# Performance work log

Measured on AMD Instinct MI355X. Metric: run time of the kernel, lower is better.

The kernel has to match this reference:

```python
import jax, jax.numpy as jnp
import numpy as np

B, SQ, SK, DK, DV = 8, 2048, 2048, 256, 256
EPS = 1e-7  # keras.backend.epsilon()


def setup_inputs() -> dict:
    key = jax.random.key(0)
    kq, kk, kv, km = jax.random.split(key, 4)
    query = jax.random.normal(kq, (B, SQ, DK), dtype=jnp.float32)
    k_ = jax.random.normal(kk, (B, SK, DK), dtype=jnp.float32)
    value = jax.random.normal(kv, (B, SK, DV), dtype=jnp.float32)
    mask = jax.random.uniform(km, (B, SK)) > 0.1
    return {"query": query, "key": k_, "value": value, "mask": mask}


def reference(query, key, value, mask):
    d = query.shape[-1]
    # scores: [B, Sq, Sk]
    e = jnp.einsum('bqd,bkd->bqk', query, key) / jnp.sqrt(jnp.asarray(d, query.dtype))
    # original applies exp(e - max) BEFORE masking (non-standard but faithful)
    e = jnp.exp(e - jnp.max(e, axis=-1, keepdims=True))
    q_len, k_len = query.shape[1], key.shape[1]
    causal = (jnp.arange(k_len)[None, :] <= jnp.arange(q_len)[:, None]).astype(query.dtype)
    e = e * causal[None, :, :]                       # history_only mask
    e = e * mask[:, None, :].astype(query.dtype)     # key padding mask
    a = e / (jnp.sum(e, axis=-1, keepdims=True) + EPS)
    return jnp.einsum('bqk,bkv->bqv', a, value)
```

## Files before the change

kernel.cpp:

```cpp
#include <hip/hip_runtime.h>
#include <hip/hip_bf16.h>

#define B_   8
#define SQ_  2048
#define SK_  2048
#define DK_  256
#define DV_  256

#define KT    32
#define PSTR  40
#define TELEM (KT * DK_)
#define NQB   16

typedef __bf16 bf16x8 __attribute__((ext_vector_type(8)));
typedef float  f32x4  __attribute__((ext_vector_type(4)));

__device__ __forceinline__ void gl_lds16(const void* g, void* l) {
    __builtin_amdgcn_global_load_lds(
        (const __attribute__((address_space(1))) void*)g,
        (__attribute__((address_space(3))) void*)l, 16, 0, 0);
}

__global__ __launch_bounds__(256)
void make_tiles(const float* __restrict__ K, const float* __restrict__ V,
                __bf16* __restrict__ Kt, __bf16* __restrict__ Vt)
{
    const int b = blockIdx.x, t = blockIdx.y;
    const float* ksrc = K + ((size_t)(b * SK_ + t * KT)) * DK_;
    const float* vsrc = V + ((size_t)(b * SK_ + t * KT)) * DV_;

    float4 kf[8];
    #pragma unroll
    for (int it = 0; it < 4; ++it) {
        int ci  = it * 256 + threadIdx.x;
        int dk8 = ci >> 5;
        int key = ci & 31;
        const float* p = ksrc + (size_t)key * DK_ + dk8 * 8;
        kf[it * 2]     = *(const float4*)(p);
        kf[it * 2 + 1] = *(const float4*)(p + 4);
    }
    const int kc8 = threadIdx.x >> 6;
    const int dv4 = threadIdx.x & 63;
    float4 vf[8];
    {
        const float* p = vsrc + (size_t)(kc8 * 8) * DV_ + dv4 * 4;
        #pragma unroll
        for (int j = 0; j < 8; ++j)
            vf[j] = *(const float4*)(p + (size_t)j * DV_);
    }

    __bf16* kout = Kt + ((size_t)(b * 64 + t)) * TELEM;
    #pragma unroll
    for (int it = 0; it < 4; ++it) {
        int ci = it * 256 + threadIdx.x;
        bf16x8 o;
        o[0] = (__bf16)kf[it*2].x;   o[1] = (__bf16)kf[it*2].y;
        o[2] = (__bf16)kf[it*2].z;   o[3] = (__bf16)kf[it*2].w;
        o[4] = (__bf16)kf[it*2+1].x; o[5] = (__bf16)kf[it*2+1].y;
        o[6] = (__bf16)kf[it*2+1].z; o[7] = (__bf16)kf[it*2+1].w;
        *(bf16x8*)(kout + (size_t)ci * 8) = o;
    }
    __bf16* vout = Vt + ((size_t)(b * 64 + t)) * TELEM;
    {
        bf16x8 o0, o1, o2, o3;
        #pragma unroll
        for (int j = 0; j < 8; ++j) {
            o0[j] = (__bf16)vf[j].x; o1[j] = (__bf16)vf[j].y;
            o2[j] = (__bf16)vf[j].z; o3[j] = (__bf16)vf[j].w;
        }
        __bf16* q = vout + (size_t)(kc8 * 256 + dv4 * 4) * 8;
        *(bf16x8*)(q)      = o0;
        *(bf16x8*)(q + 8)  = o1;
        *(bf16x8*)(q + 16) = o2;
        *(bf16x8*)(q + 24) = o3;
    }
}

__global__ __launch_bounds__(256, 2)
void attn_fwd(const float* __restrict__ Qg, const __bf16* __restrict__ Kt,
              const __bf16* __restrict__ Vt, const void* __restrict__ Mv,
              __bf16* __restrict__ Opart, float* __restrict__ Lpart,
              float* __restrict__ Og, int tpc, int slots_pb)
{
    __shared__ __align__(16) __bf16 sK[2][TELEM];
    __shared__ __align__(16) __bf16 sV[2][TELEM];
    __shared__ __align__(16) __bf16 sP[4][32 * PSTR];

    const int tid  = threadIdx.x;
    const int wv   = tid >> 6;
    const int lane = tid & 63;
    const int quad = lane >> 4;
    const int l16  = lane & 15;

    const int b = blockIdx.x;

    int yy = blockIdx.y, qb = 0, s = 0, soff = 0;
    for (int q = NQB - 1; q >= 0; --q) {
        int c = (4 * (q + 1) + tpc - 1) / tpc;
        if (yy < c) { qb = q; s = yy; break; }
        yy -= c;
        if (c > 1) soff += c;
    }
    const int nt = 4 * (qb + 1);
    const int nc = (nt + tpc - 1) / tpc;
    const int t0 = nt * s / nc;
    const int t1 = nt * (s + 1) / nc;

    const int qrow = qb * 128 + wv * 32;

    const unsigned char* Mb = (const unsigned char*)Mv;
    const int*           Mi = (const int*)Mv;
    int nzb = 0;
    {
        const unsigned int* mw = (const unsigned int*)Mv;
        #pragma unroll
        for (int i = 0; i < 32; ++i) {
            unsigned int w = mw[i];
            nzb += ((w & 0x000000ffu) != 0) + ((w & 0x0000ff00u) != 0)
                 + ((w & 0x00ff0000u) != 0) + ((w & 0xff000000u) != 0);
        }
    }
    const bool mask_byte = (nzb > 40);

    bf16x8 qfrag[2][8];
    #pragma unroll
    for (int rs = 0; rs < 2; ++rs) {
        const float* qp = Qg + ((size_t)(b * SQ_ + qrow + rs * 16 + l16)) * DK_ + quad * 8;
        #pragma unroll
        for (int kt = 0; kt < 8; ++kt) {
            float4 f0 = *(const float4*)(qp + kt * 32);
            float4 f1 = *(const float4*)(qp + kt * 32 + 4);
            bf16x8 q;
            q[0] = (__bf16)f0.x; q[1] = (__bf16)f0.y; q[2] = (__bf16)f0.z; q[3] = (__bf16)f0.w;
            q[4] = (__bf16)f1.x; q[5] = (__bf16)f1.y; q[6] = (__bf16)f1.z; q[7] = (__bf16)f1.w;
            qfrag[rs][kt] = q;
        }
    }

    f32x4 oacc[2][16];
    #pragma unroll
    for (int rs = 0; rs < 2; ++rs)
        #pragma unroll
        for (int v = 0; v < 16; ++v) oacc[rs][v] = (f32x4){0.f, 0.f, 0.f, 0.f};
    float lsum[2][4] = {{0.f,0.f,0.f,0.f},{0.f,0.f,0.f,0.f}};

    const __bf16* Kbase = Kt + (size_t)b * 64 * TELEM;
    const __bf16* Vbase = Vt + (size_t)b * 64 * TELEM;
    const size_t  mbase = (size_t)b * SK_;

    {
        const __bf16* kg = Kbase + (size_t)t0 * TELEM;
        const __bf16* vg = Vbase + (size_t)t0 * TELEM;
        #pragma unroll
        for (int r = 0; r < 4; ++r) {
            int ci = r * 256 + tid;
            gl_lds16(kg + (size_t)ci * 8, (char*)&sK[0][0] + ci * 16);
            gl_lds16(vg + (size_t)ci * 8, (char*)&sV[0][0] + ci * 16);
        }
    }
    __syncthreads();

    int cur = 0;
    for (int t = t0; t < t1; ++t) {
        if (t + 1 < t1) {
            const __bf16* kg = Kbase + (size_t)(t + 1) * TELEM;
            const __bf16* vg = Vbase + (size_t)(t + 1) * TELEM;
            #pragma unroll
            for (int r = 0; r < 4; ++r) {
                int ci = r * 256 + tid;
                gl_lds16(kg + (size_t)ci * 8, (char*)&sK[cur ^ 1][0] + ci * 16);
                gl_lds16(vg + (size_t)ci * 8, (char*)&sV[cur ^ 1][0] + ci * 16);
            }
        }

        const int k0 = t * KT;

        f32x4 s00 = {0.f,0.f,0.f,0.f}, s01 = {0.f,0.f,0.f,0.f};
        f32x4 s10 = {0.f,0.f,0.f,0.f}, s11 = {0.f,0.f,0.f,0.f};
        __builtin_amdgcn_s_setprio(1);
        #pragma unroll
        for (int kt = 0; kt < 8; ++kt) {
            bf16x8 b0 = *(const bf16x8*)&sK[cur][(size_t)((kt * 4 + quad) * 32 + l16)      * 8];
            bf16x8 b1 = *(const bf16x8*)&sK[cur][(size_t)((kt * 4 + quad) * 32 + 16 + l16) * 8];
            s00 = __builtin_amdgcn_mfma_f32_16x16x32_bf16(qfrag[0][kt], b0, s00, 0, 0, 0);
            s01 = __builtin_amdgcn_mfma_f32_16x16x32_bf16(qfrag[0][kt], b1, s01, 0, 0, 0);
            s10 = __builtin_amdgcn_mfma_f32_16x16x32_bf16(qfrag[1][kt], b0, s10, 0, 0, 0);
            s11 = __builtin_amdgcn_mfma_f32_16x16x32_bf16(qfrag[1][kt], b1, s11, 0, 0, 0);
        }
        __builtin_amdgcn_s_setprio(0);

        #pragma unroll
        for (int nf = 0; nf < 2; ++nf) {
            int key = k0 + nf * 16 + l16;
            float mk = mask_byte ? (Mb[mbase + key] ? 1.0f : 0.0f)
                                 : (Mi[mbase + key] ? 1.0f : 0.0f);
            #pragma unroll
            for (int rs = 0; rs < 2; ++rs) {
                f32x4 sv = (rs == 0) ? ((nf == 0) ? s00 : s01)
                                     : ((nf == 0) ? s10 : s11);
                #pragma unroll
                for (int i = 0; i < 4; ++i) {
                    int qr = qrow + rs * 16 + quad * 4 + i;
                    float p = __expf(sv[i] * 0.0625f);
                    p = (key <= qr) ? (p * mk) : 0.0f;
                    lsum[rs][i] += p;
                    sP[wv][(rs * 16 + quad * 4 + i) * PSTR + nf * 16 + l16] = (__bf16)p;
                }
            }
        }
        asm volatile("s_waitcnt lgkmcnt(0)" ::: "memory");
        __builtin_amdgcn_wave_barrier();

        {
            bf16x8 pa0 = *(const bf16x8*)&sP[wv][(l16)      * PSTR + quad * 8];
            bf16x8 pa1 = *(const bf16x8*)&sP[wv][(16 + l16) * PSTR + quad * 8];
            __builtin_amdgcn_s_setprio(1);
            #pragma unroll
            for (int vf = 0; vf < 16; ++vf) {
                bf16x8 bv = *(const bf16x8*)&sV[cur][(size_t)(quad * 256 + vf * 16 + l16) * 8];
                oacc[0][vf] = __builtin_amdgcn_mfma_f32_16x16x32_bf16(pa0, bv, oacc[0][vf], 0, 0, 0);
                oacc[1][vf] = __builtin_amdgcn_mfma_f32_16x16x32_bf16(pa1, bv, oacc[1][vf], 0, 0, 0);
            }
            __builtin_amdgcn_s_setprio(0);
        }

        __syncthreads();
        cur ^= 1;
    }

    #pragma unroll
    for (int rs = 0; rs < 2; ++rs)
        #pragma unroll
        for (int i = 0; i < 4; ++i) {
            float v = lsum[rs][i];
            v += __shfl_xor(v, 1);
            v += __shfl_xor(v, 2);
            v += __shfl_xor(v, 4);
            v += __shfl_xor(v, 8);
            lsum[rs][i] = v;
        }

    if (nc == 1) {
        float* op = Og + ((size_t)(b * SQ_ + qb * 128 + wv * 32)) * DV_;
        #pragma unroll
        for (int rs = 0; rs < 2; ++rs)
            #pragma unroll
            for (int i = 0; i < 4; ++i) {
                float inv = 1.0f / (lsum[rs][i] + 1e-7f);
                #pragma unroll
                for (int vf = 0; vf < 16; ++vf)
                    op[(size_t)(rs * 16 + quad * 4 + i) * DV_ + vf * 16 + l16]
                        = oacc[rs][vf][i] * inv;
            }
        return;
    }

    const size_t slot = (size_t)b * slots_pb + soff + s;
    if (l16 == 0) {
        #pragma unroll
        for (int rs = 0; rs < 2; ++rs)
            #pragma unroll
            for (int i = 0; i < 4; ++i)
                Lpart[slot * 128 + wv * 32 + rs * 16 + quad * 4 + i] = lsum[rs][i];
    }
    __bf16* ob = Opart + slot * (size_t)(128 * 256);
    #pragma unroll
    for (int rs = 0; rs < 2; ++rs)
        #pragma unroll
        for (int vf = 0; vf < 16; ++vf)
            #pragma unroll
            for (int i = 0; i < 4; ++i)
                ob[(wv * 32 + rs * 16 + quad * 4 + i) * 256 + vf * 16 + l16]
                    = (__bf16)oacc[rs][vf][i];
}

__global__ __launch_bounds__(512)
void attn_reduce(const __bf16* __restrict__ Opart, const float* __restrict__ Lpart,
                 float* __restrict__ Og, int tpc, int slots_pb)
{
    const int b    = blockIdx.x;
    const int y    = blockIdx.y;
    const int qb64 = y >> 1;
    const int half = y & 1;
    const int qb   = qb64 >> 1;
    const int rowbase = (qb64 & 1) * 64;
    const int chunks = (4 * (qb + 1) + tpc - 1) / tpc;
    if (chunks < 2) return;

    int soff = 0;
    for (int q = NQB - 1; q > qb; --q) {
        int c = (4 * (q + 1) + tpc - 1) / tpc;
        if (c > 1) soff += c;
    }

    const int tid  = threadIdx.x;
    const int row  = tid >> 3;
    const int cg   = tid & 7;

    const size_t sbase = (size_t)b * slots_pb + soff;
    float acc[16];
    #pragma unroll
    for (int i = 0; i < 16; ++i) acc[i] = 0.f;
    float ls = 0.f;

    for (int s = 0; s < chunks; ++s) {
        const __bf16* p = Opart + (sbase + s) * (size_t)(128 * 256)
                        + (size_t)(rowbase + row) * 256 + half * 128 + cg * 16;
        bf16x8 x0 = *(const bf16x8*)(p);
        bf16x8 x1 = *(const bf16x8*)(p + 8);
        #pragma unroll
        for (int e = 0; e < 8; ++e) { acc[e] += (float)x0[e]; acc[8 + e] += (float)x1[e]; }
        ls += Lpart[(sbase + s) * 128 + rowbase + row];
    }
    const float inv = 1.0f / (ls + 1e-7f);
    float* op = Og + ((size_t)b * SQ_ + qb64 * 64 + row) * DV_ + half * 128 + cg * 16;
    #pragma unroll
    for (int v = 0; v < 4; ++v) {
        float4 o;
        o.x = acc[v * 4 + 0] * inv; o.y = acc[v * 4 + 1] * inv;
        o.z = acc[v * 4 + 2] * inv; o.w = acc[v * 4 + 3] * inv;
        *(float4*)(op + v * 4) = o;
    }
}

extern "C" void kernel_launch(void* const* d_in, const int* in_sizes, int n_in,
                              void* d_out, int out_size, void* d_ws, size_t ws_size,
                              hipStream_t stream) {
    const float* Q = (const float*)d_in[0];
    const float* K = (const float*)d_in[1];
    const float* V = (const float*)d_in[2];
    const void*  M = d_in[3];
    float* Out = (float*)d_out;

    __bf16* Ktl = (__bf16*)d_ws;
    __bf16* Vtl = Ktl + (size_t)B_ * 64 * TELEM;
    __bf16* Opart = Vtl + (size_t)B_ * 64 * TELEM;

    auto counts = [](int tpc, int& nch, int& slots_pb) {
        nch = 0; slots_pb = 0;
        for (int q = 0; q < NQB; ++q) {
            int c = (4 * (q + 1) + tpc - 1) / tpc;
            nch += c;
            if (c > 1) slots_pb += c;
        }
    };
    int tpc = 10, nch, slots_pb;
    counts(tpc, nch, slots_pb);
    size_t need = (size_t)(16 * 1024 * 1024)
                + (size_t)B_ * slots_pb * (128 * 256) * 2
                + (size_t)B_ * slots_pb * 128 * 4;
    if (ws_size < need) {
        tpc = 64;
        counts(tpc, nch, slots_pb);
    }

    float* Lpart = (float*)(Opart + (size_t)B_ * slots_pb * (128 * 256));

    make_tiles<<<dim3(B_, 64), dim3(256), 0, stream>>>(K, V, Ktl, Vtl);
    attn_fwd<<<dim3(B_, nch), dim3(256), 0, stream>>>(Q, Ktl, Vtl, M, Opart, Lpart,
                                                      Out, tpc, slots_pb);
    if (slots_pb > 0)
        attn_reduce<<<dim3(B_, 64), dim3(512), 0, stream>>>(Opart, Lpart, Out,
                                                            tpc, slots_pb);
}
```

Before: 139.3 us.

## Skip fully masked causal tiles per wave and transpose QK MFMA output layout

Each wave now skips the QK, softmax and PV work for key tiles lying entirely above its causal diagonal. The QK MFMA operands are swapped so every lane holds four consecutive keys for one query row. This lets the mask be read as a vector load, lets P be written to LDS as packed bf16x4 stores, and shrinks the row-sum reduction to two shuffles. The work split across blocks is unchanged, so skipped tiles can leave waves within a block imbalanced while they still wait at the shared barrier.

```diff
diff --git a/kernel.cpp b/kernel.cpp
--- a/kernel.cpp
+++ b/kernel.cpp
@@ -13,6 +13,7 @@
 #define NQB   16
 
 typedef __bf16 bf16x8 __attribute__((ext_vector_type(8)));
+typedef __bf16 bf16x4 __attribute__((ext_vector_type(4)));
 typedef float  f32x4  __attribute__((ext_vector_type(4)));
 
 __device__ __forceinline__ void gl_lds16(const void* g, void* l) {
@@ -121,6 +122,7 @@
         }
     }
     const bool mask_byte = (nzb > 40);
+    const size_t mbase = (size_t)b * SK_;
 
     bf16x8 qfrag[2][8];
     #pragma unroll
@@ -142,11 +144,10 @@
     for (int rs = 0; rs < 2; ++rs)
         #pragma unroll
         for (int v = 0; v < 16; ++v) oacc[rs][v] = (f32x4){0.f, 0.f, 0.f, 0.f};
-    float lsum[2][4] = {{0.f,0.f,0.f,0.f},{0.f,0.f,0.f,0.f}};
+    float lsum[2] = {0.f, 0.f};
 
     const __bf16* Kbase = Kt + (size_t)b * 64 * TELEM;
     const __bf16* Vbase = Vt + (size_t)b * 64 * TELEM;
-    const size_t  mbase = (size_t)b * SK_;
 
     {
         const __bf16* kg = Kbase + (size_t)t0 * TELEM;
@@ -175,53 +176,65 @@
 
         const int k0 = t * KT;
 
-        f32x4 s00 = {0.f,0.f,0.f,0.f}, s01 = {0.f,0.f,0.f,0.f};
-        f32x4 s10 = {0.f,0.f,0.f,0.f}, s11 = {0.f,0.f,0.f,0.f};
-        __builtin_amdgcn_s_setprio(1);
-        #pragma unroll
-        for (int kt = 0; kt < 8; ++kt) {
-            bf16x8 b0 = *(const bf16x8*)&sK[cur][(size_t)((kt * 4 + quad) * 32 + l16)      * 8];
-            bf16x8 b1 = *(const bf16x8*)&sK[cur][(size_t)((kt * 4 + quad) * 32 + 16 + l16) * 8];
-            s00 = __builtin_amdgcn_mfma_f32_16x16x32_bf16(qfrag[0][kt], b0, s00, 0, 0, 0);
-            s01 = __builtin_amdgcn_mfma_f32_16x16x32_bf16(qfrag[0][kt], b1, s01, 0, 0, 0);
-            s10 = __builtin_amdgcn_mfma_f32_16x16x32_bf16(qfrag[1][kt], b0, s10, 0, 0, 0);
-            s11 = __builtin_amdgcn_mfma_f32_16x16x32_bf16(qfrag[1][kt], b1, s11, 0, 0, 0);
-        }
-        __builtin_amdgcn_s_setprio(0);
-
-        #pragma unroll
-        for (int nf = 0; nf < 2; ++nf) {
-            int key = k0 + nf * 16 + l16;
-            float mk = mask_byte ? (Mb[mbase + key] ? 1.0f : 0.0f)
-                                 : (Mi[mbase + key] ? 1.0f : 0.0f);
-            #pragma unroll
-            for (int rs = 0; rs < 2; ++rs) {
-                f32x4 sv = (rs == 0) ? ((nf == 0) ? s00 : s01)
-                                     : ((nf == 0) ? s10 : s11);
+        if (k0 <= qrow + 31) {
+            f32x4 s00 = {0.f,0.f,0.f,0.f}, s01 = {0.f,0.f,0.f,0.f};
+            f32x4 s10 = {0.f,0.f,0.f,0.f}, s11 = {0.f,0.f,0.f,0.f};
+            __builtin_amdgcn_s_setprio(1);
+            #pragma unroll
+            for (int kt = 0; kt < 8; ++kt) {
+                bf16x8 b0 = *(const bf16x8*)&sK[cur][(size_t)((kt * 4 + quad) * 32 + l16)      * 8];
+                bf16x8 b1 = *(const bf16x8*)&sK[cur][(size_t)((kt * 4 + quad) * 32 + 16 + l16) * 8];
+                s00 = __builtin_amdgcn_mfma_f32_16x16x32_bf16(b0, qfrag[0][kt], s00, 0, 0, 0);
+                s10 = __builtin_amdgcn_mfma_f32_16x16x32_bf16(b1, qfrag[0][kt], s10, 0, 0, 0);
+                s01 = __builtin_amdgcn_mfma_f32_16x16x32_bf16(b0, qfrag[1][kt], s01, 0, 0, 0);
+                s11 = __builtin_amdgcn_mfma_f32_16x16x32_bf16(b1, qfrag[1][kt], s11, 0, 0, 0);
+            }
+            __builtin_amdgcn_s_setprio(0);
+
+            #pragma unroll
+            for (int kh = 0; kh < 2; ++kh) {
+                const int kbase = k0 + kh * 16 + quad * 4;
+                float mk[4];
+                if (mask_byte) {
+                    uchar4 m4 = *(const uchar4*)(Mb + mbase + kbase);
+                    mk[0] = m4.x ? 1.f : 0.f; mk[1] = m4.y ? 1.f : 0.f;
+                    mk[2] = m4.z ? 1.f : 0.f; mk[3] = m4.w ? 1.f : 0.f;
+                } else {
+                    int4 m4 = *(const int4*)(Mi + mbase + kbase);
+                    mk[0] = m4.x ? 1.f : 0.f; mk[1] = m4.y ? 1.f : 0.f;
+                    mk[2] = m4.z ? 1.f : 0.f; mk[3] = m4.w ? 1.f : 0.f;
+                }
                 #pragma unroll
-                for (int i = 0; i < 4; ++i) {
-                    int qr = qrow + rs * 16 + quad * 4 + i;
-                    float p = __expf(sv[i] * 0.0625f);
-                    p = (key <= qr) ? (p * mk) : 0.0f;
-                    lsum[rs][i] += p;
-                    sP[wv][(rs * 16 + quad * 4 + i) * PSTR + nf * 16 + l16] = (__bf16)p;
+                for (int rs = 0; rs < 2; ++rs) {
+                    f32x4 sv = (rs == 0) ? ((kh == 0) ? s00 : s10)
+                                         : ((kh == 0) ? s01 : s11);
+                    const int qr = qrow + rs * 16 + l16;
+                    bf16x4 pv4;
+                    #pragma unroll
+                    for (int i = 0; i < 4; ++i) {
+                        float p = __expf(sv[i] * 0.0625f);
+                        p = (kbase + i <= qr) ? (p * mk[i]) : 0.0f;
+                        lsum[rs] += p;
+                        pv4[i] = (__bf16)p;
+                    }
+                    *(bf16x4*)&sP[wv][(rs * 16 + l16) * PSTR + kh * 16 + quad * 4] = pv4;
                 }
             }
-        }
-        asm volatile("s_waitcnt lgkmcnt(0)" ::: "memory");
-        __builtin_amdgcn_wave_barrier();
-
-        {
-            bf16x8 pa0 = *(const bf16x8*)&sP[wv][(l16)      * PSTR + quad * 8];
-            bf16x8 pa1 = *(const bf16x8*)&sP[wv][(16 + l16) * PSTR + quad * 8];
-            __builtin_amdgcn_s_setprio(1);
-            #pragma unroll
-            for (int vf = 0; vf < 16; ++vf) {
-                bf16x8 bv = *(const bf16x8*)&sV[cur][(size_t)(quad * 256 + vf * 16 + l16) * 8];
-                oacc[0][vf] = __builtin_amdgcn_mfma_f32_16x16x32_bf16(pa0, bv, oacc[0][vf], 0, 0, 0);
-                oacc[1][vf] = __builtin_amdgcn_mfma_f32_16x16x32_bf16(pa1, bv, oacc[1][vf], 0, 0, 0);
-            }
-            __builtin_amdgcn_s_setprio(0);
+            asm volatile("s_waitcnt lgkmcnt(0)" ::: "memory");
+            __builtin_amdgcn_wave_barrier();
+
+            {
+                bf16x8 pa0 = *(const bf16x8*)&sP[wv][(l16)      * PSTR + quad * 8];
+                bf16x8 pa1 = *(const bf16x8*)&sP[wv][(16 + l16) * PSTR + quad * 8];
+                __builtin_amdgcn_s_setprio(1);
+                #pragma unroll
+                for (int vf = 0; vf < 16; ++vf) {
+                    bf16x8 bv = *(const bf16x8*)&sV[cur][(size_t)(quad * 256 + vf * 16 + l16) * 8];
+                    oacc[0][vf] = __builtin_amdgcn_mfma_f32_16x16x32_bf16(pa0, bv, oacc[0][vf], 0, 0, 0);
+                    oacc[1][vf] = __builtin_amdgcn_mfma_f32_16x16x32_bf16(pa1, bv, oacc[1][vf], 0, 0, 0);
+                }
+                __builtin_amdgcn_s_setprio(0);
+            }
         }
 
         __syncthreads();
@@ -229,16 +242,12 @@
     }
 
     #pragma unroll
-    for (int rs = 0; rs < 2; ++rs)
-        #pragma unroll
-        for (int i = 0; i < 4; ++i) {
-            float v = lsum[rs][i];
-            v += __shfl_xor(v, 1);
-            v += __shfl_xor(v, 2);
-            v += __shfl_xor(v, 4);
-            v += __shfl_xor(v, 8);
-            lsum[rs][i] = v;
-        }
+    for (int rs = 0; rs < 2; ++rs) {
+        float v = lsum[rs];
+        v += __shfl_xor(v, 16);
+        v += __shfl_xor(v, 32);
+        lsum[rs] = v;
+    }
 
     if (nc == 1) {
         float* op = Og + ((size_t)(b * SQ_ + qb * 128 + wv * 32)) * DV_;
@@ -246,7 +255,8 @@
         for (int rs = 0; rs < 2; ++rs)
             #pragma unroll
             for (int i = 0; i < 4; ++i) {
-                float inv = 1.0f / (lsum[rs][i] + 1e-7f);
+                float ls  = __shfl(lsum[rs], quad * 4 + i);
+                float inv = 1.0f / (ls + 1e-7f);
                 #pragma unroll
                 for (int vf = 0; vf < 16; ++vf)
                     op[(size_t)(rs * 16 + quad * 4 + i) * DV_ + vf * 16 + l16]
@@ -256,12 +266,10 @@
     }
 
     const size_t slot = (size_t)b * slots_pb + soff + s;
-    if (l16 == 0) {
+    if (quad == 0) {
         #pragma unroll
         for (int rs = 0; rs < 2; ++rs)
-            #pragma unroll
-            for (int i = 0; i < 4; ++i)
-                Lpart[slot * 128 + wv * 32 + rs * 16 + quad * 4 + i] = lsum[rs][i];
+            Lpart[slot * 128 + wv * 32 + rs * 16 + l16] = lsum[rs];
     }
     __bf16* ob = Opart + slot * (size_t)(128 * 256);
     #pragma unroll
```

New measurement: 137.5 us. Within noise of the previous version (-1.3%).
